# Kernel optimization log

Hardware: AMD Instinct MI355X
Metric: run time of the kernel (lower is better)

## Reference

```python
import jax, jax.numpy as jnp
import numpy as np


def _conv_valid(x, w):
    # x: [B, Cin, H, W], w: [Cout, Cin, K, K], stride 1, no padding
    return jax.lax.conv_general_dilated(
        x, w, window_strides=(1, 1), padding='VALID',
        dimension_numbers=('NCHW', 'OIHW', 'NCHW'))


def _buggy_maxpool(x, k=2):
    # Faithful to the source MaxPool: window of size kxk slides with STRIDE 1,
    # but only the first H//k x W//k positions are kept (top-left region).
    nh = x.shape[2] // k
    nw = x.shape[3] // k
    m = jax.lax.reduce_window(
        x, -jnp.inf, jax.lax.max,
        window_dimensions=(1, 1, k, k),
        window_strides=(1, 1, 1, 1),
        padding='VALID')  # [B, C, H-k+1, W-k+1]
    return m[:, :, :nh, :nw]


def setup_inputs() -> dict:
    key = jax.random.key(0)
    ks = jax.random.split(key, 9)
    B = 8192
    x = jax.random.normal(ks[0], (B, 3, 32, 32), dtype=jnp.float32)
    s = 0.1
    conv1_w = jax.random.normal(ks[1], (6, 3, 5, 5), dtype=jnp.float32) * s
    conv2_w = jax.random.normal(ks[2], (16, 6, 5, 5), dtype=jnp.float32) * s
    fc1_w = jax.random.normal(ks[3], (120, 400), dtype=jnp.float32) * s
    fc1_b = jax.random.normal(ks[4], (120,), dtype=jnp.float32) * s
    fc2_w = jax.random.normal(ks[5], (84, 120), dtype=jnp.float32) * s
    fc2_b = jax.random.normal(ks[6], (84,), dtype=jnp.float32) * s
    fc3_w = jax.random.normal(ks[7], (10, 84), dtype=jnp.float32) * s
    fc3_b = jax.random.normal(ks[8], (10,), dtype=jnp.float32) * s
    return {
        'x': x,
        'conv1_w': conv1_w, 'conv2_w': conv2_w,
        'fc1_w': fc1_w, 'fc1_b': fc1_b,
        'fc2_w': fc2_w, 'fc2_b': fc2_b,
        'fc3_w': fc3_w, 'fc3_b': fc3_b,
    }


def reference(x, conv1_w, conv2_w, fc1_w, fc1_b, fc2_w, fc2_b, fc3_w, fc3_b):
    h = _buggy_maxpool(jax.nn.relu(_conv_valid(x, conv1_w)))   # [B,6,14,14]
    h = _buggy_maxpool(jax.nn.relu(_conv_valid(h, conv2_w)))   # [B,16,5,5]
    h = h.reshape(-1, 16 * 5 * 5)                              # [B,400]
    h = jax.nn.relu(h @ fc1_w.T + fc1_b)                       # [B,120]
    h = jax.nn.relu(h @ fc2_w.T + fc2_b)                       # [B,84]
    return h @ fc3_w.T + fc3_b                                 # [B,10]
```

## Files before the change

### kernel.cpp

```cpp
#include <hip/hip_runtime.h>


typedef float v2f __attribute__((ext_vector_type(2)));
__device__ __forceinline__ v2f mk2(float a, float b) { v2f t; t.x = a; t.y = b; return t; }
__device__ __forceinline__ v2f shfl2(v2f v, int src) {
    v2f r; r.x = __shfl(v.x, src, 64); r.y = __shfl(v.y, src, 64); return r;
}

constexpr int THREADS = 512;
constexpr int IPB = 16;

constexpr int W1P_OFF = 0;
constexpr int W2P_OFF = 452;
constexpr int IMG_BASE = 2852;
constexpr int XS_OFF = 0;
constexpr int P1_OFF = 0;
constexpr int P2_OFF = 0;
constexpr int SCR_OFF = 400;
constexpr int F1_OFF = 0;
constexpr int F2_OFF = 128;
constexpr int IMG_STRIDE = 900;
constexpr int LDS_FLOATS = IMG_BASE + IPB * IMG_STRIDE;

__device__ __forceinline__ void wave_sync() {
    asm volatile("s_waitcnt lgkmcnt(0)" ::: "memory");
}

extern "C" __global__ __launch_bounds__(THREADS, 8)
void lenet_fused(const float* __restrict__ x,
                 const float* __restrict__ w1,
                 const float* __restrict__ w2,
                 const float* __restrict__ fc1w, const float* __restrict__ fc1b,
                 const float* __restrict__ fc2w, const float* __restrict__ fc2b,
                 const float* __restrict__ fc3w, const float* __restrict__ fc3b,
                 float* __restrict__ out)
{
    __shared__ __align__(16) float lds[LDS_FLOATS];
    const int tid  = threadIdx.x;
    const int lane = tid & 63;
    const int wv   = tid >> 6;
    const int img0 = blockIdx.x * IPB;
    const v2f zero2 = mk2(0.f, 0.f);

    for (int i = tid; i < 450; i += THREADS) {
        int ocp = i / 150, rem = i - ocp * 150, k = rem >> 1, h = rem & 1;
        lds[W1P_OFF + i] = w1[(2 * ocp + h) * 75 + k];
    }
    for (int i = tid; i < 2400; i += THREADS) {
        int ocp = i / 300, rem = i - ocp * 300, k = rem >> 1, h = rem & 1;
        lds[W2P_OFF + i] = w2[(2 * ocp + h) * 150 + k];
    }

    float* baseA = lds + IMG_BASE + (wv * 2) * IMG_STRIDE;
    float* baseB = baseA + IMG_STRIDE;
    {
        const float4* xgA = (const float4*)(x + (size_t)(img0 + wv * 2) * 3072);
        const float4* xgB = (const float4*)(x + (size_t)(img0 + wv * 2 + 1) * 3072);
        float4* dA = (float4*)(baseA + XS_OFF);
        float4* dB = (float4*)(baseB + XS_OFF);
        for (int i = lane; i < 180; i += 64) {
            int c = i / 60, rem = i - c * 60;
            int r = rem >> 2, c4 = rem & 3;
            int dst = c * 75 + r * 5 + c4;
            int src = c * 256 + r * 8 + c4;
            dA[dst] = xgA[src];
            dB[dst] = xgB[src];
        }
    }
    __syncthreads();

    float* p1A = baseA + P1_OFF;
    float* p1B = baseB + P1_OFF;

    {
        const int l   = (lane < 33) ? lane : 32;
        const int ocp = l / 11;
        const int r   = l - ocp * 11;
        const float4* xsA = (const float4*)(baseA + XS_OFF);
        const float4* xsB = (const float4*)(baseB + XS_OFF);
        const v2f* w1p = (const v2f*)(lds + W1P_OFF);

        v2f accA[11], accB[11];
        #pragma unroll
        for (int c = 0; c < 11; ++c) { accA[c] = zero2; accB[c] = zero2; }

        #pragma unroll
        for (int i = 0; i < 15; ++i) {
            const int ci = i / 5, kr = i - ci * 5;
            const int b = ci * 75 + (r + kr) * 5;
            float4 A0 = xsA[b], A1 = xsA[b + 1], A2 = xsA[b + 2], A3 = xsA[b + 3];
            float4 B0 = xsB[b], B1 = xsB[b + 1], B2 = xsB[b + 2], B3 = xsB[b + 3];
            v2f W[5];
            #pragma unroll
            for (int kc = 0; kc < 5; ++kc) W[kc] = w1p[ocp * 75 + i * 5 + kc];
            float xa[16], xb[16];
            xa[0]=A0.x; xa[1]=A0.y; xa[2]=A0.z;  xa[3]=A0.w;
            xa[4]=A1.x; xa[5]=A1.y; xa[6]=A1.z;  xa[7]=A1.w;
            xa[8]=A2.x; xa[9]=A2.y; xa[10]=A2.z; xa[11]=A2.w;
            xa[12]=A3.x; xa[13]=A3.y; xa[14]=A3.z; xa[15]=A3.w;
            xb[0]=B0.x; xb[1]=B0.y; xb[2]=B0.z;  xb[3]=B0.w;
            xb[4]=B1.x; xb[5]=B1.y; xb[6]=B1.z;  xb[7]=B1.w;
            xb[8]=B2.x; xb[9]=B2.y; xb[10]=B2.z; xb[11]=B2.w;
            xb[12]=B3.x; xb[13]=B3.y; xb[14]=B3.z; xb[15]=B3.w;
            #pragma unroll
            for (int kc = 0; kc < 5; ++kc) {
                #pragma unroll
                for (int c = 0; c < 11; ++c) {
                    accA[c] = __builtin_elementwise_fma(
                        mk2(xa[c + kc], xa[c + kc]), W[kc], accA[c]);
                    accB[c] = __builtin_elementwise_fma(
                        mk2(xb[c + kc], xb[c + kc]), W[kc], accB[c]);
                }
            }
        }

        v2f pmA[10], pmB[10], mA[10], mB[10];
        #pragma unroll
        for (int c = 0; c < 10; ++c) {
            v2f aA0 = __builtin_elementwise_max(accA[c], zero2);
            v2f aA1 = __builtin_elementwise_max(accA[c + 1], zero2);
            pmA[c] = __builtin_elementwise_max(aA0, aA1);
            v2f aB0 = __builtin_elementwise_max(accB[c], zero2);
            v2f aB1 = __builtin_elementwise_max(accB[c + 1], zero2);
            pmB[c] = __builtin_elementwise_max(aB0, aB1);
        }
        #pragma unroll
        for (int c = 0; c < 10; ++c) {
            mA[c] = __builtin_elementwise_max(pmA[c], shfl2(pmA[c], lane + 1));
            mB[c] = __builtin_elementwise_max(pmB[c], shfl2(pmB[c], lane + 1));
        }
        wave_sync();
        if (r < 10) {
            const int oc0 = ocp * 2;
            float2* dA0 = (float2*)(p1A + oc0 * 120 + r * 12);
            float2* dA1 = (float2*)(p1A + (oc0 + 1) * 120 + r * 12);
            float2* dB0 = (float2*)(p1B + oc0 * 120 + r * 12);
            float2* dB1 = (float2*)(p1B + (oc0 + 1) * 120 + r * 12);
            #pragma unroll
            for (int j = 0; j < 5; ++j) {
                dA0[j] = make_float2(mA[2 * j].x, mA[2 * j + 1].x);
                dA1[j] = make_float2(mA[2 * j].y, mA[2 * j + 1].y);
                dB0[j] = make_float2(mB[2 * j].x, mB[2 * j + 1].x);
                dB1[j] = make_float2(mB[2 * j].y, mB[2 * j + 1].y);
            }
        }
    }
    wave_sync();

    float* p2A = baseA + P2_OFF;
    float* p2B = baseB + P2_OFF;
    {
        const int l   = (lane < 48) ? lane : 47;
        const int ocp = l / 6;
        const int r   = l - ocp * 6;
        const float4* pA4 = (const float4*)p1A;
        const float2* pA2 = (const float2*)p1A;
        const float4* pB4 = (const float4*)p1B;
        const float2* pB2 = (const float2*)p1B;
        const v2f* w2p = (const v2f*)(lds + W2P_OFF);

        v2f accA[6], accB[6];
        #pragma unroll
        for (int c = 0; c < 6; ++c) { accA[c] = zero2; accB[c] = zero2; }

        #pragma unroll
        for (int i = 0; i < 30; ++i) {
            const int ci = i / 5, kr = i - ci * 5;
            float4 A0 = pA4[ci * 30 + (r + kr) * 3 + 0];
            float4 A1 = pA4[ci * 30 + (r + kr) * 3 + 1];
            float2 A2 = pA2[ci * 60 + (r + kr) * 6 + 4];
            float4 B0 = pB4[ci * 30 + (r + kr) * 3 + 0];
            float4 B1 = pB4[ci * 30 + (r + kr) * 3 + 1];
            float2 B2 = pB2[ci * 60 + (r + kr) * 6 + 4];
            v2f W[5];
            #pragma unroll
            for (int kc = 0; kc < 5; ++kc) W[kc] = w2p[ocp * 150 + i * 5 + kc];
            float xa[10], xb[10];
            xa[0]=A0.x; xa[1]=A0.y; xa[2]=A0.z; xa[3]=A0.w;
            xa[4]=A1.x; xa[5]=A1.y; xa[6]=A1.z; xa[7]=A1.w;
            xa[8]=A2.x; xa[9]=A2.y;
            xb[0]=B0.x; xb[1]=B0.y; xb[2]=B0.z; xb[3]=B0.w;
            xb[4]=B1.x; xb[5]=B1.y; xb[6]=B1.z; xb[7]=B1.w;
            xb[8]=B2.x; xb[9]=B2.y;
            #pragma unroll
            for (int kc = 0; kc < 5; ++kc) {
                #pragma unroll
                for (int c = 0; c < 6; ++c) {
                    accA[c] = __builtin_elementwise_fma(
                        mk2(xa[c + kc], xa[c + kc]), W[kc], accA[c]);
                    accB[c] = __builtin_elementwise_fma(
                        mk2(xb[c + kc], xb[c + kc]), W[kc], accB[c]);
                }
            }
        }

        v2f pmA[5], pmB[5], mA[5], mB[5];
        #pragma unroll
        for (int c = 0; c < 5; ++c) {
            v2f aA0 = __builtin_elementwise_max(accA[c], zero2);
            v2f aA1 = __builtin_elementwise_max(accA[c + 1], zero2);
            pmA[c] = __builtin_elementwise_max(aA0, aA1);
            v2f aB0 = __builtin_elementwise_max(accB[c], zero2);
            v2f aB1 = __builtin_elementwise_max(accB[c + 1], zero2);
            pmB[c] = __builtin_elementwise_max(aB0, aB1);
        }
        #pragma unroll
        for (int c = 0; c < 5; ++c) {
            mA[c] = __builtin_elementwise_max(pmA[c], shfl2(pmA[c], lane + 1));
            mB[c] = __builtin_elementwise_max(pmB[c], shfl2(pmB[c], lane + 1));
        }
        wave_sync();
        if (r < 5) {
            const int oc0 = ocp * 2;
            #pragma unroll
            for (int c = 0; c < 5; ++c) {
                p2A[oc0 * 25 + r * 5 + c]       = mA[c].x;
                p2A[(oc0 + 1) * 25 + r * 5 + c] = mA[c].y;
                p2B[oc0 * 25 + r * 5 + c]       = mB[c].x;
                p2B[(oc0 + 1) * 25 + r * 5 + c] = mB[c].y;
            }
        }
    }
    __syncthreads();

    if (tid < 480) {
        const int row  = tid >> 2;
        const int rh   = tid & 3;
        const int half = rh >> 1;
        const int imh  = rh & 1;
        const float4* wrow = (const float4*)(fc1w + row * 400) + half * 50;
        #pragma unroll
        for (int pass = 0; pass < 2; ++pass) {
            const int ib = pass * 8 + imh * 4;
            v2f acc[4];
            #pragma unroll
            for (int q = 0; q < 4; ++q) acc[q] = zero2;
            #pragma unroll 2
            for (int k = 0; k < 50; ++k) {
                float4 w4 = wrow[k];
                const v2f wxy = mk2(w4.x, w4.y), wzw = mk2(w4.z, w4.w);
                #pragma unroll
                for (int q = 0; q < 4; ++q) {
                    const float4* ap = (const float4*)(lds + IMG_BASE + (ib + q) * IMG_STRIDE + P2_OFF) + half * 50;
                    float4 a = ap[k];
                    acc[q] = __builtin_elementwise_fma(mk2(a.x, a.y), wxy, acc[q]);
                    acc[q] = __builtin_elementwise_fma(mk2(a.z, a.w), wzw, acc[q]);
                }
            }
            #pragma unroll
            for (int q = 0; q < 4; ++q)
                lds[IMG_BASE + (ib + q) * IMG_STRIDE + SCR_OFF + row * 2 + half] =
                    acc[q].x + acc[q].y;
        }
    }
    __syncthreads();

    if (tid < 120) {
        const float b = fc1b[tid];
        #pragma unroll
        for (int im = 0; im < 16; ++im) {
            const float* s = lds + IMG_BASE + im * IMG_STRIDE + SCR_OFF;
            float v = s[tid * 2] + s[tid * 2 + 1] + b;
            lds[IMG_BASE + im * IMG_STRIDE + F1_OFF + tid] = fmaxf(v, 0.f);
        }
    }
    __syncthreads();

    if (tid < 168) {
        const int row = tid >> 1;
        const int imh = tid & 1;
        const float4* wrow = (const float4*)(fc2w + row * 120);
        const float bz = fc2b[row];
        #pragma unroll
        for (int pass = 0; pass < 2; ++pass) {
            const int ib = pass * 8 + imh * 4;
            v2f acc[4];
            #pragma unroll
            for (int q = 0; q < 4; ++q) acc[q] = zero2;
            #pragma unroll 2
            for (int k = 0; k < 30; ++k) {
                float4 w4 = wrow[k];
                const v2f wxy = mk2(w4.x, w4.y), wzw = mk2(w4.z, w4.w);
                #pragma unroll
                for (int q = 0; q < 4; ++q) {
                    const float4* fp = (const float4*)(lds + IMG_BASE + (ib + q) * IMG_STRIDE + F1_OFF);
                    float4 a = fp[k];
                    acc[q] = __builtin_elementwise_fma(mk2(a.x, a.y), wxy, acc[q]);
                    acc[q] = __builtin_elementwise_fma(mk2(a.z, a.w), wzw, acc[q]);
                }
            }
            #pragma unroll
            for (int q = 0; q < 4; ++q)
                lds[IMG_BASE + (ib + q) * IMG_STRIDE + F2_OFF + row] =
                    fmaxf(acc[q].x + acc[q].y + bz, 0.f);
        }
    }
    __syncthreads();

    if (tid < 160) {
        const int im  = tid / 10;
        const int row = tid - im * 10;
        const float4* wrow = (const float4*)(fc3w + row * 84);
        const float4* f2 = (const float4*)(lds + IMG_BASE + im * IMG_STRIDE + F2_OFF);
        v2f acc = zero2;
        #pragma unroll
        for (int k = 0; k < 21; ++k) {
            float4 w4 = wrow[k];
            float4 a = f2[k];
            acc = __builtin_elementwise_fma(mk2(a.x, a.y), mk2(w4.x, w4.y), acc);
            acc = __builtin_elementwise_fma(mk2(a.z, a.w), mk2(w4.z, w4.w), acc);
        }
        out[(size_t)(img0 + im) * 10 + row] = acc.x + acc.y + fc3b[row];
    }
}

extern "C" void kernel_launch(void* const* d_in, const int* in_sizes, int n_in,
                              void* d_out, int out_size, void* d_ws, size_t ws_size,
                              hipStream_t stream) {
    const float* x    = (const float*)d_in[0];
    const float* w1   = (const float*)d_in[1];
    const float* w2   = (const float*)d_in[2];
    const float* fc1w = (const float*)d_in[3];
    const float* fc1b = (const float*)d_in[4];
    const float* fc2w = (const float*)d_in[5];
    const float* fc2b = (const float*)d_in[6];
    const float* fc3w = (const float*)d_in[7];
    const float* fc3b = (const float*)d_in[8];
    float* out = (float*)d_out;

    const int B = in_sizes[0] / 3072;
    const int grid = B / IPB;
    lenet_fused<<<grid, THREADS, 0, stream>>>(x, w1, w2, fc1w, fc1b,
                                              fc2w, fc2b, fc3w, fc3b, out);
}
```

Measured before the change: 209.9 us.

## Register-tile fc1 and fc2 as 4x4 output blocks with split-K partial sums

fc1 is reorganized so each thread computes a 4-row by 4-image register tile over a quarter of K, writing four partial sums per output that a second pass reduces with bias and ReLU across all 480 threads. fc2 similarly uses 4x4 register tiles over 84 threads instead of 168 threads doing 4 images twice. This raises arithmetic intensity per LDS/global load and cuts redundant weight reads, at the cost of more registers and fewer active threads in fc2. Scalar FMAs replace packed v2f FMAs, which may lose dual-issue throughput.

```diff
diff --git a/kernel.cpp b/kernel.cpp
--- a/kernel.cpp
+++ b/kernel.cpp
@@ -224,75 +224,83 @@
     __syncthreads();
 
     if (tid < 480) {
-        const int row  = tid >> 2;
-        const int rh   = tid & 3;
-        const int half = rh >> 1;
-        const int imh  = rh & 1;
-        const float4* wrow = (const float4*)(fc1w + row * 400) + half * 50;
-        #pragma unroll
-        for (int pass = 0; pass < 2; ++pass) {
-            const int ib = pass * 8 + imh * 4;
-            v2f acc[4];
-            #pragma unroll
-            for (int q = 0; q < 4; ++q) acc[q] = zero2;
-            #pragma unroll 2
-            for (int k = 0; k < 50; ++k) {
-                float4 w4 = wrow[k];
-                const v2f wxy = mk2(w4.x, w4.y), wzw = mk2(w4.z, w4.w);
-                #pragma unroll
-                for (int q = 0; q < 4; ++q) {
-                    const float4* ap = (const float4*)(lds + IMG_BASE + (ib + q) * IMG_STRIDE + P2_OFF) + half * 50;
-                    float4 a = ap[k];
-                    acc[q] = __builtin_elementwise_fma(mk2(a.x, a.y), wxy, acc[q]);
-                    acc[q] = __builtin_elementwise_fma(mk2(a.z, a.w), wzw, acc[q]);
-                }
-            }
+        const int rq  = tid >> 4;
+        const int kq  = (tid >> 2) & 3;
+        const int imq = tid & 3;
+        const float4* ap0 = (const float4*)(lds + IMG_BASE + (imq * 4 + 0) * IMG_STRIDE + P2_OFF) + kq * 25;
+        const float4* ap1 = (const float4*)(lds + IMG_BASE + (imq * 4 + 1) * IMG_STRIDE + P2_OFF) + kq * 25;
+        const float4* ap2 = (const float4*)(lds + IMG_BASE + (imq * 4 + 2) * IMG_STRIDE + P2_OFF) + kq * 25;
+        const float4* ap3 = (const float4*)(lds + IMG_BASE + (imq * 4 + 3) * IMG_STRIDE + P2_OFF) + kq * 25;
+        const float* wb = fc1w + (rq * 4) * 400 + kq * 100;
+        float acc[4][4];
+        #pragma unroll
+        for (int q = 0; q < 4; ++q)
+            #pragma unroll
+            for (int s = 0; s < 4; ++s) acc[q][s] = 0.f;
+        for (int j = 0; j < 25; ++j) {
+            float4 a0 = ap0[j], a1 = ap1[j], a2 = ap2[j], a3 = ap3[j];
+            #pragma unroll
+            for (int s = 0; s < 4; ++s) {
+                float4 w4 = *(const float4*)(wb + s * 400 + j * 4);
+                acc[0][s] += a0.x*w4.x + a0.y*w4.y + a0.z*w4.z + a0.w*w4.w;
+                acc[1][s] += a1.x*w4.x + a1.y*w4.y + a1.z*w4.z + a1.w*w4.w;
+                acc[2][s] += a2.x*w4.x + a2.y*w4.y + a2.z*w4.z + a2.w*w4.w;
+                acc[3][s] += a3.x*w4.x + a3.y*w4.y + a3.z*w4.z + a3.w*w4.w;
+            }
+        }
+        #pragma unroll
+        for (int q = 0; q < 4; ++q)
+            #pragma unroll
+            for (int s = 0; s < 4; ++s)
+                lds[IMG_BASE + (imq * 4 + q) * IMG_STRIDE + SCR_OFF + (rq * 4 + s) * 4 + kq] = acc[q][s];
+    }
+    __syncthreads();
+
+    if (tid < 480) {
+        const int row = tid >> 2;
+        const int imq = tid & 3;
+        const float b = fc1b[row];
+        #pragma unroll
+        for (int q = 0; q < 4; ++q) {
+            const int im = imq * 4 + q;
+            float4 s4 = *(const float4*)(lds + IMG_BASE + im * IMG_STRIDE + SCR_OFF + row * 4);
+            float v = (s4.x + s4.y) + (s4.z + s4.w) + b;
+            lds[IMG_BASE + im * IMG_STRIDE + F1_OFF + row] = fmaxf(v, 0.f);
+        }
+    }
+    __syncthreads();
+
+    if (tid < 84) {
+        const int rq  = tid >> 2;
+        const int imq = tid & 3;
+        const float4* fp0 = (const float4*)(lds + IMG_BASE + (imq * 4 + 0) * IMG_STRIDE + F1_OFF);
+        const float4* fp1 = (const float4*)(lds + IMG_BASE + (imq * 4 + 1) * IMG_STRIDE + F1_OFF);
+        const float4* fp2 = (const float4*)(lds + IMG_BASE + (imq * 4 + 2) * IMG_STRIDE + F1_OFF);
+        const float4* fp3 = (const float4*)(lds + IMG_BASE + (imq * 4 + 3) * IMG_STRIDE + F1_OFF);
+        const float* wb = fc2w + (rq * 4) * 120;
+        float acc[4][4];
+        #pragma unroll
+        for (int q = 0; q < 4; ++q)
+            #pragma unroll
+            for (int s = 0; s < 4; ++s) acc[q][s] = 0.f;
+        for (int j = 0; j < 30; ++j) {
+            float4 a0 = fp0[j], a1 = fp1[j], a2 = fp2[j], a3 = fp3[j];
+            #pragma unroll
+            for (int s = 0; s < 4; ++s) {
+                float4 w4 = *(const float4*)(wb + s * 120 + j * 4);
+                acc[0][s] += a0.x*w4.x + a0.y*w4.y + a0.z*w4.z + a0.w*w4.w;
+                acc[1][s] += a1.x*w4.x + a1.y*w4.y + a1.z*w4.z + a1.w*w4.w;
+                acc[2][s] += a2.x*w4.x + a2.y*w4.y + a2.z*w4.z + a2.w*w4.w;
+                acc[3][s] += a3.x*w4.x + a3.y*w4.y + a3.z*w4.z + a3.w*w4.w;
+            }
+        }
+        #pragma unroll
+        for (int s = 0; s < 4; ++s) {
+            const float bz = fc2b[rq * 4 + s];
             #pragma unroll
             for (int q = 0; q < 4; ++q)
-                lds[IMG_BASE + (ib + q) * IMG_STRIDE + SCR_OFF + row * 2 + half] =
-                    acc[q].x + acc[q].y;
-        }
-    }
-    __syncthreads();
-
-    if (tid < 120) {
-        const float b = fc1b[tid];
-        #pragma unroll
-        for (int im = 0; im < 16; ++im) {
-            const float* s = lds + IMG_BASE + im * IMG_STRIDE + SCR_OFF;
-            float v = s[tid * 2] + s[tid * 2 + 1] + b;
-            lds[IMG_BASE + im * IMG_STRIDE + F1_OFF + tid] = fmaxf(v, 0.f);
-        }
-    }
-    __syncthreads();
-
-    if (tid < 168) {
-        const int row = tid >> 1;
-        const int imh = tid & 1;
-        const float4* wrow = (const float4*)(fc2w + row * 120);
-        const float bz = fc2b[row];
-        #pragma unroll
-        for (int pass = 0; pass < 2; ++pass) {
-            const int ib = pass * 8 + imh * 4;
-            v2f acc[4];
-            #pragma unroll
-            for (int q = 0; q < 4; ++q) acc[q] = zero2;
-            #pragma unroll 2
-            for (int k = 0; k < 30; ++k) {
-                float4 w4 = wrow[k];
-                const v2f wxy = mk2(w4.x, w4.y), wzw = mk2(w4.z, w4.w);
-                #pragma unroll
-                for (int q = 0; q < 4; ++q) {
-                    const float4* fp = (const float4*)(lds + IMG_BASE + (ib + q) * IMG_STRIDE + F1_OFF);
-                    float4 a = fp[k];
-                    acc[q] = __builtin_elementwise_fma(mk2(a.x, a.y), wxy, acc[q]);
-                    acc[q] = __builtin_elementwise_fma(mk2(a.z, a.w), wzw, acc[q]);
-                }
-            }
-            #pragma unroll
-            for (int q = 0; q < 4; ++q)
-                lds[IMG_BASE + (ib + q) * IMG_STRIDE + F2_OFF + row] =
-                    fmaxf(acc[q].x + acc[q].y + bz, 0.f);
+                lds[IMG_BASE + (imq * 4 + q) * IMG_STRIDE + F2_OFF + rq * 4 + s] =
+                    fmaxf(acc[q][s] + bz, 0.f);
         }
     }
     __syncthreads();
```

Result: slower. 222.1 us (+5.8%).
